# Performance work log

Hardware: AMD Instinct MI355X
Metric: run time of the kernel (lower is better)

## Reference

```python
import jax, jax.numpy as jnp
import numpy as np

B, N, D = 4096, 128, 256


def setup_inputs() -> dict:
    key = jax.random.key(0)
    ks = jax.random.split(key, 6)
    return {
        "label": jax.random.normal(ks[0], (B, N, D), dtype=jnp.float32),
        "adj_in": jax.random.uniform(ks[1], (N, N), dtype=jnp.float32),
        "adj_out": jax.random.uniform(ks[2], (N, N), dtype=jnp.float32),
        "edge_bias": jnp.zeros((N, D), dtype=jnp.float32),
        "gate_weight": jax.random.normal(ks[3], (D, 1), dtype=jnp.float32) * (6.0 / (D + 1)) ** 0.5,
        "bias_gate": jnp.zeros((N, 1), dtype=jnp.float32),
        "out_edge_bias": jnp.zeros((N, D), dtype=jnp.float32),
        "out_gate_weight": jax.random.normal(ks[4], (D, 1), dtype=jnp.float32) * (6.0 / (D + 1)) ** 0.5,
        "out_bias_gate": jnp.zeros((N, 1), dtype=jnp.float32),
        "loop_gate": jax.random.normal(ks[5], (D, 1), dtype=jnp.float32) * (6.0 / (D + 1)) ** 0.5,
    }


def reference(label, adj_in, adj_out, edge_bias, gate_weight, bias_gate,
              out_edge_bias, out_gate_weight, out_bias_gate, loop_gate):
    h = label  # [B, N, D]
    # origin_adj is a constant buffer in the original module (detached numpy)
    origin = jax.lax.stop_gradient(jnp.where(adj_in <= 0, adj_in, 1.0))

    # in-arc branch: masked dense adjacency matmul + bias + scalar gate
    h_in = jnp.einsum('mn,bnd->bmd', origin * adj_in, h)            # [B, N, D]
    in_gate = jnp.einsum('bnd,do->bno', h, gate_weight) + bias_gate  # [B, N, 1]
    msg_in = (h_in + edge_bias) * jax.nn.sigmoid(in_gate)

    # out-arc branch: transposed mask times out adjacency
    h_out = jnp.einsum('mn,bnd->bmd', origin.T * adj_out, h)
    out_gate = jnp.einsum('bnd,do->bno', h, out_gate_weight) + out_bias_gate
    msg_out = (h_out + out_edge_bias) * jax.nn.sigmoid(out_gate)

    # self-loop branch
    lp_gate = jnp.einsum('bnd,do->bno', h, loop_gate)
    msg_loop = h * jax.nn.sigmoid(lp_gate)

    # dropout p=0.0 -> identity
    return jax.nn.relu(msg_in + msg_out + msg_loop)
```

## Files before the change

kernel.cpp:

```cpp
#include <hip/hip_runtime.h>
#include <hip/hip_bf16.h>

#define NN 128
#define ND 256

typedef __attribute__((ext_vector_type(8))) short short8v;
typedef __attribute__((ext_vector_type(4))) short short4v;
typedef __attribute__((ext_vector_type(4))) float floatx4;

__device__ __forceinline__ unsigned short f2bf(float x){
  unsigned u = __float_as_uint(x);
  u += 0x7FFF + ((u >> 16) & 1);
  return (unsigned short)(u >> 16);
}
__device__ __forceinline__ float bf2f(unsigned short h){
  return __uint_as_float(((unsigned)h) << 16);
}

__global__ void prep_A(const float* __restrict__ adj_in, const float* __restrict__ adj_out,
                       unsigned short* __restrict__ Abf){
  int idx = blockIdx.x * 256 + threadIdx.x;
  int m = idx >> 7, n = idx & 127;
  float v;
  if (m < NN){
    float a = adj_in[m * NN + n];
    v = (a <= 0.f) ? a * a : a;
  } else {
    int mm = m - NN;
    float t = adj_in[n * NN + mm];
    float o = (t <= 0.f) ? t : 1.f;
    v = o * adj_out[mm * NN + n];
  }
  Abf[idx] = f2bf(v);
}

__global__ __launch_bounds__(512) void gcn_main(
    const float* __restrict__ H, const unsigned short* __restrict__ Abf,
    const float* __restrict__ eb,  const float* __restrict__ gw,
    const float* __restrict__ bg,  const float* __restrict__ oeb,
    const float* __restrict__ ogw, const float* __restrict__ obg,
    const float* __restrict__ lw,  float* __restrict__ Out)
{
  __shared__ __align__(16) unsigned short Ht[ND * NN];
  __shared__ float sigS[3 * NN];

  const int tid  = threadIdx.x;
  const int wave = tid >> 6;
  const int lane = tid & 63;
  const int g    = lane >> 4;
  const int m16  = lane & 15;
  const int b    = blockIdx.x;
  const float* Hb = H   + (size_t)b * NN * ND;
  float*       Ob = Out + (size_t)b * NN * ND;

  for (int pi = 0; pi < 2; ++pi){
    int p = 8 * wave + 4 * pi + g;
    int n = 2 * p;
    float s0=0.f,s1=0.f,s2=0.f,s3=0.f,s4=0.f,s5=0.f;
    #pragma unroll
    for (int di = 0; di < 8; ++di){
      int d = 32 * di + 2 * m16;
      float2 a  = *(const float2*)(Hb + n * ND + d);
      float2 c  = *(const float2*)(Hb + (n + 1) * ND + d);
      float2 w0 = *(const float2*)(gw  + d);
      float2 w1 = *(const float2*)(ogw + d);
      float2 w2 = *(const float2*)(lw  + d);
      s0 += a.x * w0.x + a.y * w0.y;
      s1 += a.x * w1.x + a.y * w1.y;
      s2 += a.x * w2.x + a.y * w2.y;
      s3 += c.x * w0.x + c.y * w0.y;
      s4 += c.x * w1.x + c.y * w1.y;
      s5 += c.x * w2.x + c.y * w2.y;
      unsigned v0 = (unsigned)f2bf(a.x) | ((unsigned)f2bf(c.x) << 16);
      unsigned v1 = (unsigned)f2bf(a.y) | ((unsigned)f2bf(c.y) << 16);
      int i0 = d       * NN + (n ^ (( d      & 7) << 3));
      int i1 = (d + 1) * NN + (n ^ (((d + 1) & 7) << 3));
      *(unsigned*)&Ht[i0] = v0;
      *(unsigned*)&Ht[i1] = v1;
    }
    #pragma unroll
    for (int m = 1; m < 16; m <<= 1){
      s0 += __shfl_xor(s0, m, 64);
      s1 += __shfl_xor(s1, m, 64);
      s2 += __shfl_xor(s2, m, 64);
      s3 += __shfl_xor(s3, m, 64);
      s4 += __shfl_xor(s4, m, 64);
      s5 += __shfl_xor(s5, m, 64);
    }
    if (m16 == 0){
      float gi0 = s0 + bg[n],     go0 = s1 + obg[n];
      float gi1 = s3 + bg[n + 1], go1 = s4 + obg[n + 1];
      sigS[n]            = 1.f / (1.f + __expf(-gi0));
      sigS[NN + n]       = 1.f / (1.f + __expf(-go0));
      sigS[2 * NN + n]   = 1.f / (1.f + __expf(-s2));
      sigS[n + 1]        = 1.f / (1.f + __expf(-gi1));
      sigS[NN + n + 1]   = 1.f / (1.f + __expf(-go1));
      sigS[2 * NN + n + 1] = 1.f / (1.f + __expf(-s5));
    }
  }
  __syncthreads();

  const int mrow = 16 * wave + m16;
  float si_[4], so_[4], sl_[4];
  #pragma unroll
  for (int r = 0; r < 4; ++r){
    int mm = 16 * wave + 4 * g + r;
    si_[r] = sigS[mm];
    so_[r] = sigS[NN + mm];
    sl_[r] = sigS[2 * NN + mm];
  }

  const floatx4 zz = {0.f, 0.f, 0.f, 0.f};
  #pragma unroll
  for (int pass = 0; pass < 2; ++pass){
    const int dbase = 128 * pass;
    floatx4 acc1[8], acc2[8];
    #pragma unroll
    for (int i = 0; i < 8; ++i){ acc1[i] = zz; acc2[i] = zz; }

    #pragma unroll
    for (int k0 = 0; k0 < 128; k0 += 32){
      const int kk = k0 + 8 * g;
      short8v a1 = *(const short8v*)&Abf[ mrow        * 128 + kk];
      short8v a2 = *(const short8v*)&Abf[(128 + mrow) * 128 + kk];
      #pragma unroll
      for (int df = 0; df < 8; ++df){
        int d = dbase + 16 * df + m16;
        const short8v bv = *(const short8v*)&Ht[d * NN + (kk ^ ((d & 7) << 3))];
        acc1[df] = __builtin_amdgcn_mfma_f32_16x16x32_bf16(a1, bv, acc1[df], 0, 0, 0);
        acc2[df] = __builtin_amdgcn_mfma_f32_16x16x32_bf16(a2, bv, acc2[df], 0, 0, 0);
      }
    }

    #pragma unroll
    for (int df = 0; df < 8; ++df){
      int d  = dbase + 16 * df + m16;
      int m0 = 16 * wave + 4 * g;
      short4v hv = *(const short4v*)&Ht[d * NN + (m0 ^ ((d & 7) << 3))];
      #pragma unroll
      for (int r = 0; r < 4; ++r){
        int mm = m0 + r;
        float hl = bf2f((unsigned short)hv[r]);
        float v = acc1[df][r] * si_[r] + acc2[df][r] * so_[r] + hl * sl_[r]
                + eb [mm * ND + d] * si_[r]
                + oeb[mm * ND + d] * so_[r];
        Ob[mm * ND + d] = fmaxf(v, 0.f);
      }
    }
  }
}

extern "C" void kernel_launch(void* const* d_in, const int* in_sizes, int n_in,
                              void* d_out, int out_size, void* d_ws, size_t ws_size,
                              hipStream_t stream){
  const float* H    = (const float*)d_in[0];
  const float* ain  = (const float*)d_in[1];
  const float* aout = (const float*)d_in[2];
  const float* eb   = (const float*)d_in[3];
  const float* gwp  = (const float*)d_in[4];
  const float* bgp  = (const float*)d_in[5];
  const float* oebp = (const float*)d_in[6];
  const float* ogwp = (const float*)d_in[7];
  const float* obgp = (const float*)d_in[8];
  const float* lwp  = (const float*)d_in[9];
  unsigned short* Abf = (unsigned short*)d_ws;

  prep_A<<<128, 256, 0, stream>>>(ain, aout, Abf);
  gcn_main<<<4096, 512, 0, stream>>>(H, Abf, eb, gwp, bgp, oebp, ogwp, obgp, lwp,
                                     (float*)d_out);
}
```

Baseline: 389.9 us.

## Vectorize H staging, transpose MFMA operands for float4 epilogue stores

The staging phase now loads H as float4 over four rows per thread group and writes packed bf16 quads into the swizzled LDS tile with a new swizzle pattern. The MFMA operands are swapped so each lane holds four consecutive d columns of one output row. That lets the epilogue use vectorized float4 loads of the bias and H and nontemporal float4 stores in place of scalar strided stores. The self-loop term now reads full-precision H from global memory again instead of the bf16 LDS copy. Launch bounds add a minimum-occupancy hint, which may increase register pressure.

```diff
diff --git a/kernel.cpp b/kernel.cpp
--- a/kernel.cpp
+++ b/kernel.cpp
@@ -12,9 +12,6 @@
   unsigned u = __float_as_uint(x);
   u += 0x7FFF + ((u >> 16) & 1);
   return (unsigned short)(u >> 16);
-}
-__device__ __forceinline__ float bf2f(unsigned short h){
-  return __uint_as_float(((unsigned)h) << 16);
 }
 
 __global__ void prep_A(const float* __restrict__ adj_in, const float* __restrict__ adj_out,
@@ -34,7 +31,7 @@
   Abf[idx] = f2bf(v);
 }
 
-__global__ __launch_bounds__(512) void gcn_main(
+__global__ __launch_bounds__(512, 4) void gcn_main(
     const float* __restrict__ H, const unsigned short* __restrict__ Abf,
     const float* __restrict__ eb,  const float* __restrict__ gw,
     const float* __restrict__ bg,  const float* __restrict__ oeb,
@@ -53,62 +50,60 @@
   const float* Hb = H   + (size_t)b * NN * ND;
   float*       Ob = Out + (size_t)b * NN * ND;
 
-  for (int pi = 0; pi < 2; ++pi){
-    int p = 8 * wave + 4 * pi + g;
-    int n = 2 * p;
-    float s0=0.f,s1=0.f,s2=0.f,s3=0.f,s4=0.f,s5=0.f;
+  const int G  = 4 * wave + g;
+  const int n0 = 4 * G;
+  float sacc[12];
+  #pragma unroll
+  for (int i = 0; i < 12; ++i) sacc[i] = 0.f;
+
+  #pragma unroll
+  for (int dq = 0; dq < 4; ++dq){
+    const int d0 = 64 * dq + 4 * m16;
+    const floatx4 wa = *(const floatx4*)(gw  + d0);
+    const floatx4 wb = *(const floatx4*)(ogw + d0);
+    const floatx4 wc = *(const floatx4*)(lw  + d0);
+    floatx4 rr[4];
     #pragma unroll
-    for (int di = 0; di < 8; ++di){
-      int d = 32 * di + 2 * m16;
-      float2 a  = *(const float2*)(Hb + n * ND + d);
-      float2 c  = *(const float2*)(Hb + (n + 1) * ND + d);
-      float2 w0 = *(const float2*)(gw  + d);
-      float2 w1 = *(const float2*)(ogw + d);
-      float2 w2 = *(const float2*)(lw  + d);
-      s0 += a.x * w0.x + a.y * w0.y;
-      s1 += a.x * w1.x + a.y * w1.y;
-      s2 += a.x * w2.x + a.y * w2.y;
-      s3 += c.x * w0.x + c.y * w0.y;
-      s4 += c.x * w1.x + c.y * w1.y;
-      s5 += c.x * w2.x + c.y * w2.y;
-      unsigned v0 = (unsigned)f2bf(a.x) | ((unsigned)f2bf(c.x) << 16);
-      unsigned v1 = (unsigned)f2bf(a.y) | ((unsigned)f2bf(c.y) << 16);
-      int i0 = d       * NN + (n ^ (( d      & 7) << 3));
-      int i1 = (d + 1) * NN + (n ^ (((d + 1) & 7) << 3));
-      *(unsigned*)&Ht[i0] = v0;
-      *(unsigned*)&Ht[i1] = v1;
+    for (int ro = 0; ro < 4; ++ro)
+      rr[ro] = *(const floatx4*)(Hb + (size_t)(n0 + ro) * ND + d0);
+    #pragma unroll
+    for (int ro = 0; ro < 4; ++ro){
+      const floatx4 r = rr[ro];
+      sacc[3*ro+0] += r[0]*wa[0] + r[1]*wa[1] + r[2]*wa[2] + r[3]*wa[3];
+      sacc[3*ro+1] += r[0]*wb[0] + r[1]*wb[1] + r[2]*wb[2] + r[3]*wb[3];
+      sacc[3*ro+2] += r[0]*wc[0] + r[1]*wc[1] + r[2]*wc[2] + r[3]*wc[3];
     }
     #pragma unroll
-    for (int m = 1; m < 16; m <<= 1){
-      s0 += __shfl_xor(s0, m, 64);
-      s1 += __shfl_xor(s1, m, 64);
-      s2 += __shfl_xor(s2, m, 64);
-      s3 += __shfl_xor(s3, m, 64);
-      s4 += __shfl_xor(s4, m, 64);
-      s5 += __shfl_xor(s5, m, 64);
+    for (int j = 0; j < 4; ++j){
+      const int d = d0 + j;
+      short4v pv;
+      pv[0] = (short)f2bf(rr[0][j]);
+      pv[1] = (short)f2bf(rr[1][j]);
+      pv[2] = (short)f2bf(rr[2][j]);
+      pv[3] = (short)f2bf(rr[3][j]);
+      *(short4v*)&Ht[d * NN + (n0 ^ (((d >> 1) & 7) << 3))] = pv;
     }
-    if (m16 == 0){
-      float gi0 = s0 + bg[n],     go0 = s1 + obg[n];
-      float gi1 = s3 + bg[n + 1], go1 = s4 + obg[n + 1];
-      sigS[n]            = 1.f / (1.f + __expf(-gi0));
-      sigS[NN + n]       = 1.f / (1.f + __expf(-go0));
-      sigS[2 * NN + n]   = 1.f / (1.f + __expf(-s2));
-      sigS[n + 1]        = 1.f / (1.f + __expf(-gi1));
-      sigS[NN + n + 1]   = 1.f / (1.f + __expf(-go1));
-      sigS[2 * NN + n + 1] = 1.f / (1.f + __expf(-s5));
+  }
+  #pragma unroll
+  for (int m = 1; m < 16; m <<= 1){
+    #pragma unroll
+    for (int i = 0; i < 12; ++i) sacc[i] += __shfl_xor(sacc[i], m, 64);
+  }
+  if (m16 == 0){
+    #pragma unroll
+    for (int ro = 0; ro < 4; ++ro){
+      const int n = n0 + ro;
+      sigS[n]          = 1.f / (1.f + __expf(-(sacc[3*ro+0] + bg[n])));
+      sigS[NN + n]     = 1.f / (1.f + __expf(-(sacc[3*ro+1] + obg[n])));
+      sigS[2*NN + n]   = 1.f / (1.f + __expf(-sacc[3*ro+2]));
     }
   }
   __syncthreads();
 
   const int mrow = 16 * wave + m16;
-  float si_[4], so_[4], sl_[4];
-  #pragma unroll
-  for (int r = 0; r < 4; ++r){
-    int mm = 16 * wave + 4 * g + r;
-    si_[r] = sigS[mm];
-    so_[r] = sigS[NN + mm];
-    sl_[r] = sigS[2 * NN + mm];
-  }
+  const float si = sigS[mrow];
+  const float so = sigS[NN + mrow];
+  const float sl = sigS[2 * NN + mrow];
 
   const floatx4 zz = {0.f, 0.f, 0.f, 0.f};
   #pragma unroll
@@ -121,31 +116,32 @@
     #pragma unroll
     for (int k0 = 0; k0 < 128; k0 += 32){
       const int kk = k0 + 8 * g;
-      short8v a1 = *(const short8v*)&Abf[ mrow        * 128 + kk];
-      short8v a2 = *(const short8v*)&Abf[(128 + mrow) * 128 + kk];
+      const short8v av1 = *(const short8v*)&Abf[ mrow        * 128 + kk];
+      const short8v av2 = *(const short8v*)&Abf[(128 + mrow) * 128 + kk];
       #pragma unroll
       for (int df = 0; df < 8; ++df){
-        int d = dbase + 16 * df + m16;
-        const short8v bv = *(const short8v*)&Ht[d * NN + (kk ^ ((d & 7) << 3))];
-        acc1[df] = __builtin_amdgcn_mfma_f32_16x16x32_bf16(a1, bv, acc1[df], 0, 0, 0);
-        acc2[df] = __builtin_amdgcn_mfma_f32_16x16x32_bf16(a2, bv, acc2[df], 0, 0, 0);
+        const int d = dbase + 16 * df + m16;
+        const short8v hv = *(const short8v*)&Ht[d * NN + (kk ^ (((d >> 1) & 7) << 3))];
+        acc1[df] = __builtin_amdgcn_mfma_f32_16x16x32_bf16(hv, av1, acc1[df], 0, 0, 0);
+        acc2[df] = __builtin_amdgcn_mfma_f32_16x16x32_bf16(hv, av2, acc2[df], 0, 0, 0);
       }
     }
 
     #pragma unroll
     for (int df = 0; df < 8; ++df){
-      int d  = dbase + 16 * df + m16;
-      int m0 = 16 * wave + 4 * g;
-      short4v hv = *(const short4v*)&Ht[d * NN + (m0 ^ ((d & 7) << 3))];
+      const int dcol = dbase + 16 * df + 4 * g;
+      const floatx4 ebv  = *(const floatx4*)(eb  + mrow * ND + dcol);
+      const floatx4 oebv = *(const floatx4*)(oeb + mrow * ND + dcol);
+      const floatx4 hv4  = *(const floatx4*)(Hb  + (size_t)mrow * ND + dcol);
+      floatx4 o;
       #pragma unroll
       for (int r = 0; r < 4; ++r){
-        int mm = m0 + r;
-        float hl = bf2f((unsigned short)hv[r]);
-        float v = acc1[df][r] * si_[r] + acc2[df][r] * so_[r] + hl * sl_[r]
-                + eb [mm * ND + d] * si_[r]
-                + oeb[mm * ND + d] * so_[r];
-        Ob[mm * ND + d] = fmaxf(v, 0.f);
+        const float v = (acc1[df][r] + ebv[r]) * si
+                      + (acc2[df][r] + oebv[r]) * so
+                      + hv4[r] * sl;
+        o[r] = fmaxf(v, 0.f);
       }
+      __builtin_nontemporal_store(o, (floatx4*)(Ob + (size_t)mrow * ND + dcol));
     }
   }
 }
```

Result: slower. 446.2 us (+14.4%).
